# Kernel optimization log

Measured on AMD Instinct MI355X. Metric: run time of the kernel, lower is better.

The kernel has to match this reference:

```python
import jax, jax.numpy as jnp
import numpy as np

IMG = 1024
P0, P1 = 32, 16          # patch_size = [32, 16], P0 = 2*P1 required by stride-2 conv
C = 1                    # num_channels (must be 1 for unflatten(encoded, 1) to be valid)
N0 = (IMG // P0) ** 2    # 1024 patches at coarse scale
N1 = (IMG // P1) ** 2    # 4096 patches at fine scale
D0 = C * P0 * P0         # 1024 projection dim (coarse)
D1 = C * P1 * P1         # 256 projection dim (fine)
B = 8
BN_EPS = 1e-3            # keras BatchNormalization default
LRELU_ALPHA = 0.3        # keras LeakyReLU default


def setup_inputs() -> dict:
    key = jax.random.key(0)
    ks = jax.random.split(key, 9)
    return {
        "X": jax.random.normal(ks[0], (B, IMG, IMG, C), jnp.float32),
        "W_emb": jax.random.normal(ks[1], (N0, D0), jnp.float32) * 0.02,
        "conv_w": jax.random.normal(ks[2], (3, 3, N0, N1), jnp.float32) * 0.02,
        "conv_b": jnp.zeros((N1,), jnp.float32),
        "bn_gamma": jax.random.uniform(ks[3], (N1,), jnp.float32) + 0.5,
        "bn_beta": jax.random.normal(ks[4], (N1,), jnp.float32) * 0.1,
        "bn_mean": jax.random.normal(ks[5], (N1,), jnp.float32) * 0.1,
        "bn_var": jax.random.uniform(ks[6], (N1,), jnp.float32) + 0.5,
        "W_dense": jax.random.normal(ks[7], (D0, D0), jnp.float32) * 0.02,
        "b_dense": jnp.zeros((D0,), jnp.float32),
    }


def _patches(x, p):
    # [B,H,W,C] -> [B, (H/p)*(W/p), p, p, C]; row-major patch order, matching tf split/stack path.
    b, h, w, c = x.shape
    x = x.reshape(b, h // p, p, w // p, p, c).transpose(0, 1, 3, 2, 4, 5)
    return x.reshape(b, (h // p) * (w // p), p, p, c)


def _unpatch(x):
    # [B, n, p, p, C] -> [B, e*p, e*p, C] with e = sqrt(n); exact inverse of _patches.
    b, n, p, _, c = x.shape
    e = int(np.sqrt(n))
    x = x.reshape(b, e, e, p, p, c).transpose(0, 1, 3, 2, 4, 5)
    return x.reshape(b, e * p, e * p, c)


def reference(X, W_emb, conv_w, conv_b, bn_gamma, bn_beta, bn_mean, bn_var, W_dense, b_dense):
    b = X.shape[0]
    # fine-scale patches, flattened
    flat = _patches(X, P1).reshape(b, N1, D1)

    # positional embedding 1: positions = arange(N0) -> full embedding table
    pos1 = W_emb  # [N0, D0]

    # positional embedding 2: unflatten -> conv branch (inference: dropout = identity, BN uses moving stats)
    pe = pos1.reshape(1, N0, P0, P0, C).transpose(0, 4, 2, 3, 1).reshape(C, P0, P0, N0)  # [C,P0,P0,N0]
    y = jax.lax.conv_general_dilated(
        pe, conv_w, window_strides=(2, 2), padding='SAME',
        dimension_numbers=('NHWC', 'HWIO', 'NHWC')) + conv_b            # [C, P1, P1, N1]
    y = (y - bn_mean) * (bn_gamma / jnp.sqrt(bn_var + BN_EPS)) + bn_beta
    y = jnp.where(y > 0, y, LRELU_ALPHA * y)
    pos2 = y.reshape(1, C, P1, P1, N1).transpose(0, 4, 2, 3, 1).reshape(1, N1, D1)

    enc = flat + pos2                                                    # [B, N1, D1]
    # unflatten(.,1) -> unpatch -> repatch at coarse scale (pure reshape/transpose)
    img = _unpatch(enc.reshape(b, N1, P1, P1, 1))                        # [B, IMG, IMG, 1]
    enc = _patches(img, P0).reshape(b, N0, D0) + pos1                    # [B, N0, D0]
    return enc @ W_dense + b_dense
```

## Files before the change

### kernel.cpp

```cpp
#include <hip/hip_runtime.h>

typedef __attribute__((ext_vector_type(8))) short short8;
typedef __attribute__((ext_vector_type(4))) short short4v;
typedef __attribute__((ext_vector_type(4))) float float4v;

typedef const void __attribute__((address_space(1)))* gptr_t;
typedef void __attribute__((address_space(3)))* lptr_t;

__device__ __forceinline__ void gload_lds16(const void* g, void* l) {
    __builtin_amdgcn_global_load_lds((gptr_t)g, (lptr_t)l, 16, 0, 0);
}

__device__ __forceinline__ unsigned short f2bf(float f) {
    union { float f; unsigned int u; } v; v.f = f;
    unsigned int r = v.u + 0x7fffu + ((v.u >> 16) & 1u);
    return (unsigned short)(r >> 16);
}

__device__ __forceinline__ short8 frag_ld(const unsigned char* base, int row, int k2) {
    return *(const short8*)(base + row * 128 + (k2 ^ ((row & 7) << 4)));
}

__device__ __forceinline__ int swzB(int n) {
    return ((n ^ (n >> 3)) & 7) << 4;
}

__device__ __forceinline__ short8 frag_ldB(const unsigned char* base, int n, int k2) {
    return *(const short8*)(base + n * 128 + (k2 ^ swzB(n)));
}

__device__ __forceinline__ float4v mfma_bf16(short8 a, short8 b, float4v c) {
    return __builtin_amdgcn_mfma_f32_16x16x32_bf16(a, b, c, 0, 0, 0);
}

__global__ __launch_bounds__(256) void k_transpose_bf16(
        const float* __restrict__ in, unsigned short* __restrict__ out) {
    __shared__ float tile[32][33];
    int tx = threadIdx.x, ty = threadIdx.y;
    int x = blockIdx.x * 32 + tx;
    int ybase = blockIdx.y * 32;
#pragma unroll
    for (int j = 0; j < 4; j++)
        tile[ty + j * 8][tx] = in[(size_t)(ybase + ty + j * 8) * 1024 + x];
    __syncthreads();
    int ox = ybase + tx;
    int oybase = blockIdx.x * 32;
#pragma unroll
    for (int j = 0; j < 4; j++)
        out[(size_t)(oybase + ty + j * 8) * 1024 + ox] = f2bf(tile[tx][ty + j * 8]);
}

__global__ __launch_bounds__(256) void k_conv_gemm(
        const float* __restrict__ convw,
        const unsigned short* __restrict__ peT,
        const unsigned short* __restrict__ zerobuf,
        float* __restrict__ y_acc)
{
    __shared__ __align__(16) unsigned char ldsA[2][16384];
    __shared__ __align__(16) unsigned char ldsB[2][8192];

    const int t  = threadIdx.x;
    const int nt = blockIdx.x;
    const int mt = blockIdx.y;
    const int s  = blockIdx.z;
    const int kh = s / 3, kw = s - kh * 3;
    const int ncol0 = nt * 64;

    const int l = t & 63, w = t >> 6;
    const int wm = w >> 1, wn = w & 1;
    const int l15 = l & 15;
    const int lk2 = (l >> 4) * 16;

    float4v acc[4][2] = {};

    const unsigned short* asrc[4];
    int aok[4];
#pragma unroll
    for (int i = 0; i < 4; i++) {
        int idx = i * 256 + t;
        int r = idx >> 3, c8 = idx & 7;
        int m = mt * 128 + r;
        int oh = m >> 4, ow = m & 15;
        int ih = 2 * oh + kh, iw = 2 * ow + kw;
        bool ok = (ih < 32) && (iw < 32);
        asrc[i] = ok ? (peT + (size_t)(ih * 32 + iw) * 1024 + ((c8 ^ (r & 7)) * 8))
                     : zerobuf;
        aok[i] = ok ? ~0 : 0;
    }

    const int g = t >> 4, l16v = t & 15;
    const int bk0 = g * 4;
    const int bn0 = l16v * 4;
    const float* bbase = convw + ((size_t)s * 1024 + bk0) * 4096 + ncol0 + bn0;

    for (int tt = 0; tt < 16; ++tt) {
        const int cur = tt & 1, nxt = cur ^ 1;

        if (tt == 0) {
#pragma unroll
            for (int i = 0; i < 4; i++) {
                int idx = i * 256 + t;
                gload_lds16(asrc[i], &ldsA[0][idx * 16]);
            }
            float4v rb[4];
#pragma unroll
            for (int i = 0; i < 4; i++)
                rb[i] = *(const float4v*)(bbase + (size_t)i * 4096);
#pragma unroll
            for (int i = 0; i < 4; i++) {
                int n = bn0 + i;
                short4v v;
                v.x = (short)f2bf(rb[0][i]);
                v.y = (short)f2bf(rb[1][i]);
                v.z = (short)f2bf(rb[2][i]);
                v.w = (short)f2bf(rb[3][i]);
                *(short4v*)(&ldsB[0][n * 128 + ((bk0 * 2) ^ swzB(n))]) = v;
            }
            __syncthreads();
        }

        float4v rbn[4];
        if (tt < 15) {
            int k0n = (tt + 1) * 64;
#pragma unroll
            for (int i = 0; i < 4; i++) {
                int idx = i * 256 + t;
                gload_lds16(asrc[i] + (k0n & aok[i]), &ldsA[nxt][idx * 16]);
            }
#pragma unroll
            for (int i = 0; i < 4; i++)
                rbn[i] = *(const float4v*)(bbase + (size_t)(k0n + i) * 4096);
        }

        short8 af[4][2], bfr[2][2];
#pragma unroll
        for (int mf = 0; mf < 4; mf++)
#pragma unroll
            for (int ks = 0; ks < 2; ks++)
                af[mf][ks] = frag_ld(ldsA[cur], wm * 64 + mf * 16 + l15, ks * 64 + lk2);
#pragma unroll
        for (int nf = 0; nf < 2; nf++)
#pragma unroll
            for (int ks = 0; ks < 2; ks++)
                bfr[nf][ks] = frag_ldB(ldsB[cur], wn * 32 + nf * 16 + l15, ks * 64 + lk2);
#pragma unroll
        for (int mf = 0; mf < 4; mf++)
#pragma unroll
            for (int nf = 0; nf < 2; nf++)
#pragma unroll
                for (int ks = 0; ks < 2; ks++)
                    acc[mf][nf] = mfma_bf16(af[mf][ks], bfr[nf][ks], acc[mf][nf]);

        if (tt < 15) {
#pragma unroll
            for (int i = 0; i < 4; i++) {
                int n = bn0 + i;
                short4v v;
                v.x = (short)f2bf(rbn[0][i]);
                v.y = (short)f2bf(rbn[1][i]);
                v.z = (short)f2bf(rbn[2][i]);
                v.w = (short)f2bf(rbn[3][i]);
                *(short4v*)(&ldsB[nxt][n * 128 + ((bk0 * 2) ^ swzB(n))]) = v;
            }
        }
        __syncthreads();
    }

#pragma unroll
    for (int mf = 0; mf < 4; mf++) {
        int row = mt * 128 + wm * 64 + mf * 16 + (l >> 4) * 4;
#pragma unroll
        for (int nf = 0; nf < 2; nf++) {
            int col = ncol0 + wn * 32 + nf * 16 + l15;
#pragma unroll
            for (int r = 0; r < 4; r++)
                atomicAdd(&y_acc[(size_t)(row + r) * 4096 + col], acc[mf][nf][r]);
        }
    }
}

__global__ __launch_bounds__(256) void k_bn_pos2(
        const float* __restrict__ y_acc, const float* __restrict__ cb,
        const float* __restrict__ gamma, const float* __restrict__ beta,
        const float* __restrict__ mean, const float* __restrict__ var,
        float* __restrict__ pos2img) {
    int idx = blockIdx.x * 256 + threadIdx.x;
    int m = idx >> 12, oc = idx & 4095;
    float v = y_acc[idx] + cb[oc];
    v = (v - mean[oc]) * (gamma[oc] * rsqrtf(var[oc] + 1e-3f)) + beta[oc];
    v = v > 0.0f ? v : 0.3f * v;
    int y = ((oc >> 6) << 4) + (m >> 4);
    int x = ((oc & 63) << 4) + (m & 15);
    pos2img[y * 1024 + x] = v;
}

__global__ __launch_bounds__(256) void k_build_A(
        const float* __restrict__ X, const float* __restrict__ pos2img,
        const float* __restrict__ W_emb, unsigned short* __restrict__ Aenc) {
    int row = blockIdx.x;
    int n0 = row & 1023;
    int b  = row >> 10;
    int d0 = threadIdx.x * 4;
    int y = ((n0 >> 5) << 5) + (d0 >> 5);
    int x = ((n0 & 31) << 5) + (d0 & 31);
    size_t pix = (size_t)y * 1024 + x;
    float4v xv = *(const float4v*)(X + (size_t)b * 1048576 + pix);
    float4v pv = *(const float4v*)(pos2img + pix);
    float4v wv = *(const float4v*)(W_emb + (size_t)n0 * 1024 + d0);
    short4v o;
    o.x = (short)f2bf(xv.x + pv.x + wv.x);
    o.y = (short)f2bf(xv.y + pv.y + wv.y);
    o.z = (short)f2bf(xv.z + pv.z + wv.z);
    o.w = (short)f2bf(xv.w + pv.w + wv.w);
    *(short4v*)(Aenc + (size_t)row * 1024 + d0) = o;
}

__global__ __launch_bounds__(256) void k_final_gemm(
        const unsigned short* __restrict__ A,
        const unsigned short* __restrict__ Bt,
        const float* __restrict__ bias,
        float* __restrict__ C) {
    __shared__ __align__(16) unsigned char ldsA[16384];
    __shared__ __align__(16) unsigned char ldsB[16384];
    const int t = threadIdx.x;
    const int col0 = blockIdx.x * 128;
    const int row0 = blockIdx.y * 128;
    const int l = t & 63, w = t >> 6;
    const int wm = w >> 1, wn = w & 1;
    const int l15 = l & 15;
    const int lk2 = (l >> 4) * 16;

    float4v acc[4][4] = {};

    const unsigned short* asrc[4];
    const unsigned short* bsrc[4];
#pragma unroll
    for (int i = 0; i < 4; i++) {
        int idx = i * 256 + t;
        int r = idx >> 3, c8 = idx & 7;
        int cofs = (c8 ^ (r & 7)) * 8;
        asrc[i] = A  + (size_t)(row0 + r) * 1024 + cofs;
        bsrc[i] = Bt + (size_t)(col0 + r) * 1024 + cofs;
    }

    for (int k0 = 0; k0 < 1024; k0 += 64) {
#pragma unroll
        for (int i = 0; i < 4; i++) {
            int idx = i * 256 + t;
            gload_lds16(asrc[i] + k0, ldsA + idx * 16);
            gload_lds16(bsrc[i] + k0, ldsB + idx * 16);
        }
        __syncthreads();

        short8 af[4][2], bfr[4][2];
#pragma unroll
        for (int mf = 0; mf < 4; mf++)
#pragma unroll
            for (int ks = 0; ks < 2; ks++)
                af[mf][ks] = frag_ld(ldsA, wm * 64 + mf * 16 + l15, ks * 64 + lk2);
#pragma unroll
        for (int nf = 0; nf < 4; nf++)
#pragma unroll
            for (int ks = 0; ks < 2; ks++)
                bfr[nf][ks] = frag_ld(ldsB, wn * 64 + nf * 16 + l15, ks * 64 + lk2);
#pragma unroll
        for (int mf = 0; mf < 4; mf++)
#pragma unroll
            for (int nf = 0; nf < 4; nf++)
#pragma unroll
                for (int ks = 0; ks < 2; ks++)
                    acc[mf][nf] = mfma_bf16(af[mf][ks], bfr[nf][ks], acc[mf][nf]);
        __syncthreads();
    }

#pragma unroll
    for (int nf = 0; nf < 4; nf++) {
        int col = col0 + wn * 64 + nf * 16 + l15;
        float bv = bias[col];
#pragma unroll
        for (int mf = 0; mf < 4; mf++) {
            int row = row0 + wm * 64 + mf * 16 + (l >> 4) * 4;
#pragma unroll
            for (int r = 0; r < 4; r++)
                C[(size_t)(row + r) * 1024 + col] = acc[mf][nf][r] + bv;
        }
    }
}

extern "C" void kernel_launch(void* const* d_in, const int* in_sizes, int n_in,
                              void* d_out, int out_size, void* d_ws, size_t ws_size,
                              hipStream_t stream) {
    (void)in_sizes; (void)n_in; (void)out_size; (void)ws_size;
    const float* X       = (const float*)d_in[0];
    const float* W_emb   = (const float*)d_in[1];
    const float* conv_w  = (const float*)d_in[2];
    const float* conv_b  = (const float*)d_in[3];
    const float* gamma   = (const float*)d_in[4];
    const float* beta    = (const float*)d_in[5];
    const float* mean    = (const float*)d_in[6];
    const float* var     = (const float*)d_in[7];
    const float* W_dense = (const float*)d_in[8];
    const float* b_dense = (const float*)d_in[9];
    float* out = (float*)d_out;

    unsigned char* ws = (unsigned char*)d_ws;
    float*          y_acc   = (float*)(ws);
    unsigned short* zerobuf = (unsigned short*)(ws + (4u << 20));
    unsigned short* peT     = (unsigned short*)(ws + (8u << 20));
    unsigned short* WdT     = (unsigned short*)(ws + (10u << 20));
    float*          pos2img = (float*)(ws + (12u << 20));
    unsigned short* Aenc    = (unsigned short*)(ws + (16u << 20));

    hipMemsetAsync(y_acc, 0, (4u << 20) + 4096, stream);

    dim3 tb(32, 8);
    k_transpose_bf16<<<dim3(32, 32), tb, 0, stream>>>(W_emb, peT);
    k_transpose_bf16<<<dim3(32, 32), tb, 0, stream>>>(W_dense, WdT);
    k_conv_gemm<<<dim3(64, 2, 9), 256, 0, stream>>>(conv_w, peT, zerobuf, y_acc);
    k_bn_pos2<<<4096, 256, 0, stream>>>(y_acc, conv_b, gamma, beta, mean, var, pos2img);
    k_build_A<<<8192, 256, 0, stream>>>(X, pos2img, W_emb, Aenc);
    k_final_gemm<<<dim3(8, 64), 256, 0, stream>>>(Aenc, WdT, b_dense, out);
}
```

Before: 117.8 us.

## Deepen conv GEMM prefetch pipeline and remap blocks for XCD locality

Restructures the conv GEMM main loop so loads run two k-steps ahead, using explicit waitcnt, split barriers, sched_barriers and setprio around the MFMA block. The goal is to hide global-load latency behind the matrix math. Both GEMMs also switch to a 1D grid whose block-index remapping groups neighbouring tiles onto the same XCD, aiming for better L2 reuse. The hand-written vmcnt and lgkmcnt counts add risk: if they do not match the compiler's emitted load order, the kernel can read data before it has arrived.

```diff
diff --git a/kernel.cpp b/kernel.cpp
--- a/kernel.cpp
+++ b/kernel.cpp
@@ -59,10 +59,12 @@
     __shared__ __align__(16) unsigned char ldsA[2][16384];
     __shared__ __align__(16) unsigned char ldsB[2][8192];
 
-    const int t  = threadIdx.x;
-    const int nt = blockIdx.x;
-    const int mt = blockIdx.y;
-    const int s  = blockIdx.z;
+    const int t = threadIdx.x;
+    const int L = blockIdx.x;
+    const int ell = (L & 7) * 144 + (L >> 3);
+    const int mt = ell & 1;
+    const int nt = (ell >> 1) & 63;
+    const int s  = ell >> 7;
     const int kh = s / 3, kw = s - kh * 3;
     const int ncol0 = nt * 64;
 
@@ -93,77 +95,93 @@
     const int bn0 = l16v * 4;
     const float* bbase = convw + ((size_t)s * 1024 + bk0) * 4096 + ncol0 + bn0;
 
+    float4v rb[2][4];
+
+#pragma unroll
+    for (int i = 0; i < 4; i++)
+        gload_lds16(asrc[i], &ldsA[0][(i * 256 + t) * 16]);
+#pragma unroll
+    for (int i = 0; i < 4; i++)
+        rb[0][i] = *(const float4v*)(bbase + (size_t)i * 4096);
+    __builtin_amdgcn_sched_barrier(0);
+#pragma unroll
+    for (int i = 0; i < 4; i++)
+        gload_lds16(asrc[i] + (64 & aok[i]), &ldsA[1][(i * 256 + t) * 16]);
+#pragma unroll
+    for (int i = 0; i < 4; i++)
+        rb[1][i] = *(const float4v*)(bbase + (size_t)(64 + i) * 4096);
+    asm volatile("s_waitcnt vmcnt(8)" ::: "memory");
+    __builtin_amdgcn_sched_barrier(0);
+#pragma unroll
+    for (int i = 0; i < 4; i++) {
+        int n = bn0 + i;
+        short4v v;
+        v.x = (short)f2bf(rb[0][0][i]);
+        v.y = (short)f2bf(rb[0][1][i]);
+        v.z = (short)f2bf(rb[0][2][i]);
+        v.w = (short)f2bf(rb[0][3][i]);
+        *(short4v*)(&ldsB[0][n * 128 + ((bk0 * 2) ^ swzB(n))]) = v;
+    }
+    asm volatile("s_waitcnt lgkmcnt(0)" ::: "memory");
+    __builtin_amdgcn_s_barrier();
+
+#pragma unroll
     for (int tt = 0; tt < 16; ++tt) {
-        const int cur = tt & 1, nxt = cur ^ 1;
-
-        if (tt == 0) {
-#pragma unroll
-            for (int i = 0; i < 4; i++) {
-                int idx = i * 256 + t;
-                gload_lds16(asrc[i], &ldsA[0][idx * 16]);
-            }
-            float4v rb[4];
+        const int cur = tt & 1;
+
+        short8 af[4][2], bfr[2][2];
+#pragma unroll
+        for (int mf = 0; mf < 4; mf++)
+#pragma unroll
+            for (int ks = 0; ks < 2; ks++)
+                af[mf][ks] = frag_ld(ldsA[cur], wm * 64 + mf * 16 + l15, ks * 64 + lk2);
+#pragma unroll
+        for (int nf = 0; nf < 2; nf++)
+#pragma unroll
+            for (int ks = 0; ks < 2; ks++)
+                bfr[nf][ks] = frag_ldB(ldsB[cur], wn * 32 + nf * 16 + l15, ks * 64 + lk2);
+        asm volatile("s_waitcnt lgkmcnt(0)" ::: "memory");
+        __builtin_amdgcn_sched_barrier(0);
+        __builtin_amdgcn_s_barrier();
+
+        if (tt < 14) {
+            const int k0n = (tt + 2) * 64;
 #pragma unroll
             for (int i = 0; i < 4; i++)
-                rb[i] = *(const float4v*)(bbase + (size_t)i * 4096);
+                gload_lds16(asrc[i] + (k0n & aok[i]), &ldsA[cur][(i * 256 + t) * 16]);
+#pragma unroll
+            for (int i = 0; i < 4; i++)
+                rb[cur][i] = *(const float4v*)(bbase + (size_t)(k0n + i) * 4096);
+        }
+
+        __builtin_amdgcn_s_setprio(1);
+#pragma unroll
+        for (int mf = 0; mf < 4; mf++)
+#pragma unroll
+            for (int nf = 0; nf < 2; nf++)
+#pragma unroll
+                for (int ks = 0; ks < 2; ks++)
+                    acc[mf][nf] = mfma_bf16(af[mf][ks], bfr[nf][ks], acc[mf][nf]);
+        __builtin_amdgcn_s_setprio(0);
+
+        if (tt < 15) {
+            if (tt < 14) asm volatile("s_waitcnt vmcnt(8)" ::: "memory");
+            else         asm volatile("s_waitcnt vmcnt(0)" ::: "memory");
+            __builtin_amdgcn_sched_barrier(0);
 #pragma unroll
             for (int i = 0; i < 4; i++) {
                 int n = bn0 + i;
                 short4v v;
-                v.x = (short)f2bf(rb[0][i]);
-                v.y = (short)f2bf(rb[1][i]);
-                v.z = (short)f2bf(rb[2][i]);
-                v.w = (short)f2bf(rb[3][i]);
-                *(short4v*)(&ldsB[0][n * 128 + ((bk0 * 2) ^ swzB(n))]) = v;
+                v.x = (short)f2bf(rb[cur ^ 1][0][i]);
+                v.y = (short)f2bf(rb[cur ^ 1][1][i]);
+                v.z = (short)f2bf(rb[cur ^ 1][2][i]);
+                v.w = (short)f2bf(rb[cur ^ 1][3][i]);
+                *(short4v*)(&ldsB[cur ^ 1][n * 128 + ((bk0 * 2) ^ swzB(n))]) = v;
             }
-            __syncthreads();
-        }
-
-        float4v rbn[4];
-        if (tt < 15) {
-            int k0n = (tt + 1) * 64;
-#pragma unroll
-            for (int i = 0; i < 4; i++) {
-                int idx = i * 256 + t;
-                gload_lds16(asrc[i] + (k0n & aok[i]), &ldsA[nxt][idx * 16]);
-            }
-#pragma unroll
-            for (int i = 0; i < 4; i++)
-                rbn[i] = *(const float4v*)(bbase + (size_t)(k0n + i) * 4096);
-        }
-
-        short8 af[4][2], bfr[2][2];
-#pragma unroll
-        for (int mf = 0; mf < 4; mf++)
-#pragma unroll
-            for (int ks = 0; ks < 2; ks++)
-                af[mf][ks] = frag_ld(ldsA[cur], wm * 64 + mf * 16 + l15, ks * 64 + lk2);
-#pragma unroll
-        for (int nf = 0; nf < 2; nf++)
-#pragma unroll
-            for (int ks = 0; ks < 2; ks++)
-                bfr[nf][ks] = frag_ldB(ldsB[cur], wn * 32 + nf * 16 + l15, ks * 64 + lk2);
-#pragma unroll
-        for (int mf = 0; mf < 4; mf++)
-#pragma unroll
-            for (int nf = 0; nf < 2; nf++)
-#pragma unroll
-                for (int ks = 0; ks < 2; ks++)
-                    acc[mf][nf] = mfma_bf16(af[mf][ks], bfr[nf][ks], acc[mf][nf]);
-
-        if (tt < 15) {
-#pragma unroll
-            for (int i = 0; i < 4; i++) {
-                int n = bn0 + i;
-                short4v v;
-                v.x = (short)f2bf(rbn[0][i]);
-                v.y = (short)f2bf(rbn[1][i]);
-                v.z = (short)f2bf(rbn[2][i]);
-                v.w = (short)f2bf(rbn[3][i]);
-                *(short4v*)(&ldsB[nxt][n * 128 + ((bk0 * 2) ^ swzB(n))]) = v;
-            }
-        }
-        __syncthreads();
+            asm volatile("s_waitcnt lgkmcnt(0)" ::: "memory");
+            __builtin_amdgcn_sched_barrier(0);
+            __builtin_amdgcn_s_barrier();
+        }
     }
 
 #pragma unroll
@@ -223,8 +241,10 @@
     __shared__ __align__(16) unsigned char ldsA[16384];
     __shared__ __align__(16) unsigned char ldsB[16384];
     const int t = threadIdx.x;
-    const int col0 = blockIdx.x * 128;
-    const int row0 = blockIdx.y * 128;
+    const int L = blockIdx.x;
+    const int ell = (L & 7) * 64 + (L >> 3);
+    const int col0 = (ell & 7) * 128;
+    const int row0 = (ell >> 3) * 128;
     const int l = t & 63, w = t >> 6;
     const int wm = w >> 1, wn = w & 1;
     const int l15 = l & 15;
@@ -316,8 +336,8 @@
     dim3 tb(32, 8);
     k_transpose_bf16<<<dim3(32, 32), tb, 0, stream>>>(W_emb, peT);
     k_transpose_bf16<<<dim3(32, 32), tb, 0, stream>>>(W_dense, WdT);
-    k_conv_gemm<<<dim3(64, 2, 9), 256, 0, stream>>>(conv_w, peT, zerobuf, y_acc);
+    k_conv_gemm<<<1152, 256, 0, stream>>>(conv_w, peT, zerobuf, y_acc);
     k_bn_pos2<<<4096, 256, 0, stream>>>(y_acc, conv_b, gamma, beta, mean, var, pos2img);
     k_build_A<<<8192, 256, 0, stream>>>(X, pos2img, W_emb, Aenc);
-    k_final_gemm<<<dim3(8, 64), 256, 0, stream>>>(Aenc, WdT, b_dense, out);
-}
+    k_final_gemm<<<512, 256, 0, stream>>>(Aenc, WdT, b_dense, out);
+}
```

Measured after the change: 108.5 us. -7.9%, faster.

## Split conv GEMM K across blocks, drop double buffering, remap block order for XCDs

Applied to the files above, without the earlier changes.

The conv GEMM now splits each tap's K=1024 into two 512 halves. That doubles the grid to 2304 blocks, and partial sums are combined through the existing atomics. The LDS double buffer is replaced by a single buffer, which halves shared memory so more blocks fit per CU (launch_bounds 256,4). Both GEMMs remap the linear block index so that neighbouring tiles land on the same XCD, for better L2 reuse. The trade-offs are more atomic traffic and losing the load/compute overlap inside each block.

```diff
diff --git a/kernel.cpp b/kernel.cpp
--- a/kernel.cpp
+++ b/kernel.cpp
@@ -50,21 +50,25 @@
         out[(size_t)(oybase + ty + j * 8) * 1024 + ox] = f2bf(tile[tx][ty + j * 8]);
 }
 
-__global__ __launch_bounds__(256) void k_conv_gemm(
+__global__ __launch_bounds__(256, 4) void k_conv_gemm(
         const float* __restrict__ convw,
         const unsigned short* __restrict__ peT,
         const unsigned short* __restrict__ zerobuf,
         float* __restrict__ y_acc)
 {
-    __shared__ __align__(16) unsigned char ldsA[2][16384];
-    __shared__ __align__(16) unsigned char ldsB[2][8192];
-
-    const int t  = threadIdx.x;
-    const int nt = blockIdx.x;
-    const int mt = blockIdx.y;
-    const int s  = blockIdx.z;
+    __shared__ __align__(16) unsigned char ldsA[16384];
+    __shared__ __align__(16) unsigned char ldsB[8192];
+
+    const int t = threadIdx.x;
+    const int L = blockIdx.x;
+    const int ell = (L & 7) * 288 + (L >> 3);
+    const int mt = ell & 1;
+    const int kc = (ell >> 1) & 1;
+    const int nt = (ell >> 2) & 63;
+    const int s  = ell >> 8;
     const int kh = s / 3, kw = s - kh * 3;
     const int ncol0 = nt * 64;
+    const int kbase = kc * 512;
 
     const int l = t & 63, w = t >> 6;
     const int wm = w >> 1, wn = w & 1;
@@ -91,58 +95,41 @@
     const int g = t >> 4, l16v = t & 15;
     const int bk0 = g * 4;
     const int bn0 = l16v * 4;
-    const float* bbase = convw + ((size_t)s * 1024 + bk0) * 4096 + ncol0 + bn0;
-
-    for (int tt = 0; tt < 16; ++tt) {
-        const int cur = tt & 1, nxt = cur ^ 1;
-
-        if (tt == 0) {
-#pragma unroll
-            for (int i = 0; i < 4; i++) {
-                int idx = i * 256 + t;
-                gload_lds16(asrc[i], &ldsA[0][idx * 16]);
-            }
-            float4v rb[4];
-#pragma unroll
-            for (int i = 0; i < 4; i++)
-                rb[i] = *(const float4v*)(bbase + (size_t)i * 4096);
-#pragma unroll
-            for (int i = 0; i < 4; i++) {
-                int n = bn0 + i;
-                short4v v;
-                v.x = (short)f2bf(rb[0][i]);
-                v.y = (short)f2bf(rb[1][i]);
-                v.z = (short)f2bf(rb[2][i]);
-                v.w = (short)f2bf(rb[3][i]);
-                *(short4v*)(&ldsB[0][n * 128 + ((bk0 * 2) ^ swzB(n))]) = v;
-            }
-            __syncthreads();
-        }
-
-        float4v rbn[4];
-        if (tt < 15) {
-            int k0n = (tt + 1) * 64;
-#pragma unroll
-            for (int i = 0; i < 4; i++) {
-                int idx = i * 256 + t;
-                gload_lds16(asrc[i] + (k0n & aok[i]), &ldsA[nxt][idx * 16]);
-            }
-#pragma unroll
-            for (int i = 0; i < 4; i++)
-                rbn[i] = *(const float4v*)(bbase + (size_t)(k0n + i) * 4096);
-        }
+    const float* bbase = convw + ((size_t)s * 1024 + kbase + bk0) * 4096 + ncol0 + bn0;
+
+    for (int tt = 0; tt < 8; ++tt) {
+        const int k0 = tt * 64;
+
+#pragma unroll
+        for (int i = 0; i < 4; i++)
+            gload_lds16(asrc[i] + ((kbase + k0) & aok[i]), &ldsA[(i * 256 + t) * 16]);
+        float4v rb[4];
+#pragma unroll
+        for (int i = 0; i < 4; i++)
+            rb[i] = *(const float4v*)(bbase + (size_t)(k0 + i) * 4096);
+#pragma unroll
+        for (int i = 0; i < 4; i++) {
+            int n = bn0 + i;
+            short4v v;
+            v.x = (short)f2bf(rb[0][i]);
+            v.y = (short)f2bf(rb[1][i]);
+            v.z = (short)f2bf(rb[2][i]);
+            v.w = (short)f2bf(rb[3][i]);
+            *(short4v*)(&ldsB[n * 128 + ((bk0 * 2) ^ swzB(n))]) = v;
+        }
+        __syncthreads();
 
         short8 af[4][2], bfr[2][2];
 #pragma unroll
         for (int mf = 0; mf < 4; mf++)
 #pragma unroll
             for (int ks = 0; ks < 2; ks++)
-                af[mf][ks] = frag_ld(ldsA[cur], wm * 64 + mf * 16 + l15, ks * 64 + lk2);
+                af[mf][ks] = frag_ld(ldsA, wm * 64 + mf * 16 + l15, ks * 64 + lk2);
 #pragma unroll
         for (int nf = 0; nf < 2; nf++)
 #pragma unroll
             for (int ks = 0; ks < 2; ks++)
-                bfr[nf][ks] = frag_ldB(ldsB[cur], wn * 32 + nf * 16 + l15, ks * 64 + lk2);
+                bfr[nf][ks] = frag_ldB(ldsB, wn * 32 + nf * 16 + l15, ks * 64 + lk2);
 #pragma unroll
         for (int mf = 0; mf < 4; mf++)
 #pragma unroll
@@ -150,19 +137,6 @@
 #pragma unroll
                 for (int ks = 0; ks < 2; ks++)
                     acc[mf][nf] = mfma_bf16(af[mf][ks], bfr[nf][ks], acc[mf][nf]);
-
-        if (tt < 15) {
-#pragma unroll
-            for (int i = 0; i < 4; i++) {
-                int n = bn0 + i;
-                short4v v;
-                v.x = (short)f2bf(rbn[0][i]);
-                v.y = (short)f2bf(rbn[1][i]);
-                v.z = (short)f2bf(rbn[2][i]);
-                v.w = (short)f2bf(rbn[3][i]);
-                *(short4v*)(&ldsB[nxt][n * 128 + ((bk0 * 2) ^ swzB(n))]) = v;
-            }
-        }
         __syncthreads();
     }
 
@@ -223,8 +197,10 @@
     __shared__ __align__(16) unsigned char ldsA[16384];
     __shared__ __align__(16) unsigned char ldsB[16384];
     const int t = threadIdx.x;
-    const int col0 = blockIdx.x * 128;
-    const int row0 = blockIdx.y * 128;
+    const int L = blockIdx.x;
+    const int ell = (L & 7) * 64 + (L >> 3);
+    const int col0 = (ell & 7) * 128;
+    const int row0 = (ell >> 3) * 128;
     const int l = t & 63, w = t >> 6;
     const int wm = w >> 1, wn = w & 1;
     const int l15 = l & 15;
@@ -316,8 +292,8 @@
     dim3 tb(32, 8);
     k_transpose_bf16<<<dim3(32, 32), tb, 0, stream>>>(W_emb, peT);
     k_transpose_bf16<<<dim3(32, 32), tb, 0, stream>>>(W_dense, WdT);
-    k_conv_gemm<<<dim3(64, 2, 9), 256, 0, stream>>>(conv_w, peT, zerobuf, y_acc);
+    k_conv_gemm<<<2304, 256, 0, stream>>>(conv_w, peT, zerobuf, y_acc);
     k_bn_pos2<<<4096, 256, 0, stream>>>(y_acc, conv_b, gamma, beta, mean, var, pos2img);
     k_build_A<<<8192, 256, 0, stream>>>(X, pos2img, W_emb, Aenc);
-    k_final_gemm<<<dim3(8, 64), 256, 0, stream>>>(Aenc, WdT, b_dense, out);
-}
+    k_final_gemm<<<512, 256, 0, stream>>>(Aenc, WdT, b_dense, out);
+}
```

New measurement: 132.5 us. 12.5% more time.
